# Optimization experiments

Measured on AMD Instinct MI355X. Metric: run time of the kernel, lower is better.

The kernel has to match this reference:

```python
import jax, jax.numpy as jnp
import numpy as np

D_MODEL = 1024
STATE_DIM = 64
SEQ_L = 2048


def hippo_legs_A(N):
    n = jnp.arange(N, dtype=jnp.float32)
    two_n1 = 2.0 * n + 1.0
    sq = jnp.sqrt(two_n1[:, None] * two_n1[None, :])
    A = jnp.tril(sq, k=-1) * -1.0
    return A + jnp.diag(-(n + 1.0))


def setup_inputs() -> dict:
    key = jax.random.key(0)
    kB, kC = jax.random.split(key)
    N = STATE_DIM
    n = jnp.arange(N, dtype=jnp.float32)
    B_ref = jnp.sqrt(2.0 * n + 1.0)  # (N,)
    B = jnp.tile(B_ref[None, :], (D_MODEL, 1)) + 0.01 * jax.random.normal(kB, (D_MODEL, N), dtype=jnp.float32)
    C = 0.1 * jax.random.normal(kC, (D_MODEL, N), dtype=jnp.float32)
    D = jnp.zeros((D_MODEL,), dtype=jnp.float32)
    log_dt = jnp.log(jnp.asarray(0.1, dtype=jnp.float32))
    return {"B": B, "C": C, "D": D, "log_dt": log_dt, "L": SEQ_L}


def reference(B, C, D, log_dt, L):
    N = B.shape[1]
    A = hippo_legs_A(N)                       # (N,N) continuous-time HiPPO-LegS
    dt = jax.nn.softplus(log_dt) + 1e-06
    I = jnp.eye(N, dtype=A.dtype)
    lhs = I - 0.5 * dt * A
    rhs = I + 0.5 * dt * A
    A_bar = jnp.linalg.solve(lhs, rhs)        # (N,N) bilinear discretization
    B_bar = jnp.linalg.solve(lhs, (dt * B).T).T  # (d_model, N)
    A_bar_T = A_bar.T

    def step(x, _):
        y = jnp.sum(C * x, axis=-1)           # (d_model,)
        return x @ A_bar_T, y

    _, ys = jax.lax.scan(step, B_bar, None, length=L)  # ys: (L, d_model)
    K = ys.T                                   # (d_model, L)
    K = K.at[:, 0].add(D)
    return K[:, None, :]                       # (d_model, 1, L)
```

## Files before the change

kernel.cpp:

```cpp
#include <hip/hip_runtime.h>

typedef unsigned short ushort_t;
typedef unsigned int uint_t;
typedef short short8 __attribute__((ext_vector_type(8)));
typedef float f32x4 __attribute__((ext_vector_type(4)));

namespace {

template<int CTRL, int RM>
__device__ __forceinline__ float dpp_mov0(float v) {
  return __int_as_float(__builtin_amdgcn_update_dpp(
      0, __float_as_int(v), CTRL, RM, 0xF, false));
}
template<int CTRL, int RM>
__device__ __forceinline__ float dpp_mov1(float v) {
  return __int_as_float(__builtin_amdgcn_update_dpp(
      0x3f800000, __float_as_int(v), CTRL, RM, 0xF, false));
}

__device__ __forceinline__ float rl(float v, int k) {
  return __int_as_float(__builtin_amdgcn_readlane(__float_as_int(v), k));
}

struct Hoist {
  float cs0, cs1, cs2, cs3, cs4, cs5;
  float gs0, gs1, gs2, gs3, gs4, gs5;
  float r, inv_d, hr, alpha, k2;
};

__device__ __forceinline__ Hoist make_hoist(float dt, int n) {
  float h = 0.5f * dt, fn = (float)n;
  float r = sqrtf(2.f * fn + 1.f);
  float d = 1.f + h * (fn + 1.f);
  float inv_d = 1.f / d;
  float g = (1.f - h * fn) * inv_d;
  float c = g - 1.f;
  Hoist H;
  H.r = r; H.inv_d = inv_d; H.hr = h * r;
  H.alpha = 1.f + h * fn;
  H.k2 = r * (2.f - d) * inv_d;
#define COEF_STEP(IDX, CTRL, RM)                                        \
  H.cs##IDX = c; H.gs##IDX = g;                                         \
  { float cP = dpp_mov0<CTRL, RM>(c);                                   \
    float gP = dpp_mov1<CTRL, RM>(g);                                   \
    c = fmaf(g, cP, c); g = g * gP; }
  COEF_STEP(0, 0x111, 0xF)
  COEF_STEP(1, 0x112, 0xF)
  COEF_STEP(2, 0x114, 0xF)
  COEF_STEP(3, 0x118, 0xF)
  COEF_STEP(4, 0x142, 0xA)
  COEF_STEP(5, 0x143, 0xC)
#undef COEF_STEP
  return H;
}

__device__ __forceinline__ float abar_apply(float x, const Hoist& H) {
  float w1 = H.r * x, w2 = H.k2 * x;
#define APPLY_STEP(IDX, CTRL, RM)                                       \
  { float w1P = dpp_mov0<CTRL, RM>(w1);                                 \
    float w2P = dpp_mov0<CTRL, RM>(w2);                                 \
    w2 = fmaf(H.cs##IDX, w1P, fmaf(H.gs##IDX, w2P, w2));                \
    w1 += w1P; }
  APPLY_STEP(0, 0x111, 0xF)
  APPLY_STEP(1, 0x112, 0xF)
  APPLY_STEP(2, 0x114, 0xF)
  APPLY_STEP(3, 0x118, 0xF)
  APPLY_STEP(4, 0x142, 0xA)
  APPLY_STEP(5, 0x143, 0xC)
#undef APPLY_STEP
  float tp = dpp_mov0<0x138, 0xF>(w2);
  return H.inv_d * fmaf(-H.hr, w1 + tp, H.alpha * x);
}

template<int CTRL, int RM>
__device__ __forceinline__ void linrec_step(float& G, float& W) {
  float Wo = dpp_mov0<CTRL, RM>(W);
  float Go = dpp_mov1<CTRL, RM>(G);
  W = fmaf(G, Wo, W);
  G *= Go;
}
__device__ __forceinline__ float lhs_solve(float z, const Hoist& H) {
  float G = H.gs0, W = H.r * z * H.inv_d;
  linrec_step<0x111, 0xF>(G, W);
  linrec_step<0x112, 0xF>(G, W);
  linrec_step<0x114, 0xF>(G, W);
  linrec_step<0x118, 0xF>(G, W);
  linrec_step<0x142, 0xA>(G, W);
  linrec_step<0x143, 0xC>(G, W);
  float sp = dpp_mov0<0x138, 0xF>(W);
  return (z - H.hr * sp) * H.inv_d;
}

__device__ __forceinline__ float softplus_dt(float ldt) {
  return log1pf(expf(ldt)) + 1e-6f;
}

#define KEEP4(v) asm volatile("" : "+v"(v.x), "+v"(v.y), "+v"(v.z), "+v"(v.w))

__device__ __forceinline__ void load_row_pin(const float* __restrict__ base,
                                             float4 (&p)[16]) {
  const float4* p4 = (const float4*)base;
  #pragma unroll
  for (int q = 0; q < 16; ++q) p[q] = p4[q];
  #pragma unroll
  for (int q = 0; q < 16; ++q) KEEP4(p[q]);
}

__device__ __forceinline__ float qapply_pin(const float4 (&p)[16], float u) {
  float a0 = 0.f, a1 = 0.f, a2 = 0.f, a3 = 0.f;
  #pragma unroll
  for (int q = 0; q < 16; ++q) {
    a0 = fmaf(p[q].x, rl(u, 4 * q + 0), a0);
    a1 = fmaf(p[q].y, rl(u, 4 * q + 1), a1);
    a2 = fmaf(p[q].z, rl(u, 4 * q + 2), a2);
    a3 = fmaf(p[q].w, rl(u, 4 * q + 3), a3);
  }
  return (a0 + a1) + (a2 + a3);
}

__device__ __forceinline__ float grow_matvec(const float* __restrict__ M,
                                             float u, int lane) {
  float a0 = 0.f, a1 = 0.f, a2 = 0.f, a3 = 0.f;
  const float4* m4 = (const float4*)(M + lane * 64);
  #pragma unroll
  for (int q = 0; q < 16; ++q) {
    float4 f = m4[q];
    a0 = fmaf(f.x, rl(u, 4 * q + 0), a0);
    a1 = fmaf(f.y, rl(u, 4 * q + 1), a1);
    a2 = fmaf(f.z, rl(u, 4 * q + 2), a2);
    a3 = fmaf(f.w, rl(u, 4 * q + 3), a3);
  }
  return (a0 + a1) + (a2 + a3);
}

__device__ __forceinline__ void split_store(float v, ushort_t* Hi,
                                            ushort_t* Lo, int row, int n) {
  uint_t uv = __float_as_uint(v);
  float hf = __uint_as_float(uv & 0xFFFF0000u);
  uint_t lv = __float_as_uint(v - hf);
  int idx = (row << 6) | (((n >> 3) ^ (row & 7)) << 3) | (n & 7);
  Hi[idx] = (ushort_t)(uv >> 16);
  Lo[idx] = (ushort_t)(lv >> 16);
}

__device__ __forceinline__ int frag_off(int row, int chunk) {
  return (row << 6) | ((chunk ^ (row & 7)) << 3);
}

}

__global__ __launch_bounds__(64) void hippo_pow(const float* __restrict__ ldt_p,
                                                float* __restrict__ A32c,
                                                float* __restrict__ QROW,
                                                float* __restrict__ Q2ROW) {
  const int lane = threadIdx.x;
  const int m = blockIdx.x;
  const float dt = softplus_dt(ldt_p[0]);
  const Hoist H = make_hoist(dt, lane);
  float x = (lane == m) ? 1.f : 0.f;
  #pragma unroll 1
  for (int s = 0; s < 32; ++s) x = abar_apply(x, H);
  A32c[lane * 64 + m] = x;
  #pragma unroll 1
  for (int s = 0; s < 32; ++s) x = abar_apply(x, H);
  QROW[m * 64 + lane] = x;
  #pragma unroll 1
  for (int s = 0; s < 64; ++s) x = abar_apply(x, H);
  Q2ROW[m * 64 + lane] = x;
}

__global__ __launch_bounds__(256) void hippo_main(
    const float* __restrict__ B, const float* __restrict__ C,
    const float* __restrict__ Dv, const float* __restrict__ ldt_p,
    const float* __restrict__ A32c, const float* __restrict__ QROW,
    const float* __restrict__ Q2ROW, float* __restrict__ out) {
  __shared__ __align__(16) ushort_t Uh[32 * 64], Ulo[32 * 64];
  __shared__ __align__(16) ushort_t Vh[64 * 64], Vlo[64 * 64];
  const int d = blockIdx.x;
  const int tau = threadIdx.x;
  const int lane = tau & 63;
  const int w = tau >> 6;
  const float dt = softplus_dt(ldt_p[0]);

  if (w == 0) {
    const Hoist H = make_hoist(dt, lane);
    float v = lhs_solve(dt * B[d * 64 + lane], H);
    #pragma unroll 1
    for (int j = 0; j < 32; ++j) {
      split_store(v, Vh, Vlo, j, lane);
      if (j < 31) v = abar_apply(v, H);
    }
  } else if (w == 3) {
    const Hoist H = make_hoist(dt, lane);
    float bb = lhs_solve(dt * B[d * 64 + lane], H);
    float v = grow_matvec(A32c, bb, lane);
    #pragma unroll 1
    for (int j = 32; j < 64; ++j) {
      split_store(v, Vh, Vlo, j, lane);
      if (j < 63) v = abar_apply(v, H);
    }
  } else if (w == 1) {
    float4 p[16];
    load_row_pin(Q2ROW + lane * 64, p);
    float u = C[d * 64 + lane];
    #pragma unroll 1
    for (int a = 0; a < 16; ++a) {
      split_store(u, Uh, Ulo, 2 * a, lane);
      if (a < 15) u = qapply_pin(p, u);
    }
  } else {
    float u = grow_matvec(QROW, C[d * 64 + lane], lane);
    float4 p[16];
    load_row_pin(Q2ROW + lane * 64, p);
    #pragma unroll 1
    for (int a = 0; a < 16; ++a) {
      split_store(u, Uh, Ulo, 2 * a + 1, lane);
      if (a < 15) u = qapply_pin(p, u);
    }
  }
  __syncthreads();

  const int it = w & 1;
  const int jp = w >> 1;
  const int arow = lane & 15;
  const int kg = lane >> 4;
  f32x4 acc0 = {0.f, 0.f, 0.f, 0.f};
  f32x4 acc1 = {0.f, 0.f, 0.f, 0.f};
  const int ia = (it << 4) + arow;
  const int jv0 = (jp << 5) + arow;
  const int jv1 = jv0 + 16;
  #pragma unroll
  for (int k0 = 0; k0 < 2; ++k0) {
    const int ci = (k0 << 2) + kg;
    short8 ah = *(const short8*)&Uh[frag_off(ia, ci)];
    short8 al = *(const short8*)&Ulo[frag_off(ia, ci)];
    short8 b0h = *(const short8*)&Vh[frag_off(jv0, ci)];
    short8 b0l = *(const short8*)&Vlo[frag_off(jv0, ci)];
    short8 b1h = *(const short8*)&Vh[frag_off(jv1, ci)];
    short8 b1l = *(const short8*)&Vlo[frag_off(jv1, ci)];
    acc0 = __builtin_amdgcn_mfma_f32_16x16x32_bf16(ah, b0h, acc0, 0, 0, 0);
    acc0 = __builtin_amdgcn_mfma_f32_16x16x32_bf16(al, b0h, acc0, 0, 0, 0);
    acc0 = __builtin_amdgcn_mfma_f32_16x16x32_bf16(ah, b0l, acc0, 0, 0, 0);
    acc1 = __builtin_amdgcn_mfma_f32_16x16x32_bf16(ah, b1h, acc1, 0, 0, 0);
    acc1 = __builtin_amdgcn_mfma_f32_16x16x32_bf16(al, b1h, acc1, 0, 0, 0);
    acc1 = __builtin_amdgcn_mfma_f32_16x16x32_bf16(ah, b1l, acc1, 0, 0, 0);
  }
  #pragma unroll
  for (int r = 0; r < 4; ++r) {
    const int i = (it << 4) + (kg << 2) + r;
    const int j0 = (jp << 5) + arow;
    float y0 = acc0[r];
    if (i == 0 && j0 == 0) y0 += Dv[d];
    out[((size_t)d << 11) + (i << 6) + j0] = y0;
    out[((size_t)d << 11) + (i << 6) + j0 + 16] = acc1[r];
  }
}

extern "C" void kernel_launch(void* const* d_in, const int* in_sizes, int n_in,
                              void* d_out, int out_size, void* d_ws, size_t ws_size,
                              hipStream_t stream) {
  const float* B   = (const float*)d_in[0];
  const float* C   = (const float*)d_in[1];
  const float* Dv  = (const float*)d_in[2];
  const float* ldt = (const float*)d_in[3];
  const int d_model = in_sizes[2];
  float* A32c  = (float*)d_ws;
  float* QROW  = (float*)d_ws + 4096;
  float* Q2ROW = (float*)d_ws + 8192;
  hippo_pow<<<64, 64, 0, stream>>>(ldt, A32c, QROW, Q2ROW);
  hippo_main<<<d_model, 256, 0, stream>>>(B, C, Dv, ldt, A32c, QROW, Q2ROW,
                                          (float*)d_out);
}
```

Before: 39.62 us.

## Shorten serial power chains with more precomputed A powers and grid-synced squaring

The prep kernel now stores A^16, A^32, A^48 and A^64, and builds the higher powers (A^128, A^256) by squaring, using atomic counters as a grid-wide barrier across the 64 blocks instead of running 64 more serial steps. In the main kernel each wave then runs two independent recurrence chains of half the length, interleaved, which halves the serial dependency depth for building the V and U tiles. The cost is extra matvecs per wave, a memset launch, and a spin-wait barrier that relies on all 64 prep blocks being resident at once.

```diff
diff --git a/kernel.cpp b/kernel.cpp
--- a/kernel.cpp
+++ b/kernel.cpp
@@ -147,33 +147,66 @@
   return (row << 6) | ((chunk ^ (row & 7)) << 3);
 }
 
-}
-
-__global__ __launch_bounds__(64) void hippo_pow(const float* __restrict__ ldt_p,
-                                                float* __restrict__ A32c,
-                                                float* __restrict__ QROW,
-                                                float* __restrict__ Q2ROW) {
+__device__ __forceinline__ void wait_cnt(const uint_t* f, uint_t tgt) {
+  while (__hip_atomic_load(f, __ATOMIC_ACQUIRE, __HIP_MEMORY_SCOPE_AGENT) < tgt)
+    __builtin_amdgcn_s_sleep(8);
+}
+__device__ __forceinline__ void signal_cnt(uint_t* f, int lane) {
+  __threadfence();
+  if (lane == 0)
+    __hip_atomic_fetch_add(f, 1u, __ATOMIC_RELEASE, __HIP_MEMORY_SCOPE_AGENT);
+}
+
+}
+
+__global__ __launch_bounds__(64) void hippo_prep(
+    const float* __restrict__ ldt_p, uint_t* __restrict__ flags,
+    float* __restrict__ A16c, float* __restrict__ A32c,
+    float* __restrict__ A48c, float* __restrict__ QROW,
+    float* __restrict__ A64RM, float* __restrict__ Q2ROW,
+    float* __restrict__ Q2RM, float* __restrict__ Q4ROW) {
   const int lane = threadIdx.x;
   const int m = blockIdx.x;
   const float dt = softplus_dt(ldt_p[0]);
   const Hoist H = make_hoist(dt, lane);
   float x = (lane == m) ? 1.f : 0.f;
   #pragma unroll 1
-  for (int s = 0; s < 32; ++s) x = abar_apply(x, H);
+  for (int s = 0; s < 16; ++s) x = abar_apply(x, H);
+  A16c[lane * 64 + m] = x;
+  #pragma unroll 1
+  for (int s = 0; s < 16; ++s) x = abar_apply(x, H);
   A32c[lane * 64 + m] = x;
   #pragma unroll 1
-  for (int s = 0; s < 32; ++s) x = abar_apply(x, H);
+  for (int s = 0; s < 16; ++s) x = abar_apply(x, H);
+  A48c[lane * 64 + m] = x;
+  #pragma unroll 1
+  for (int s = 0; s < 16; ++s) x = abar_apply(x, H);
   QROW[m * 64 + lane] = x;
-  #pragma unroll 1
-  for (int s = 0; s < 64; ++s) x = abar_apply(x, H);
-  Q2ROW[m * 64 + lane] = x;
+  A64RM[lane * 64 + m] = x;
+  signal_cnt(&flags[0], lane);
+  wait_cnt(&flags[0], 64);
+  {
+    float4 p[16];
+    load_row_pin(A64RM + lane * 64, p);
+    float x2 = qapply_pin(p, x);
+    Q2ROW[m * 64 + lane] = x2;
+    Q2RM[lane * 64 + m] = x2;
+    signal_cnt(&flags[1], lane);
+    wait_cnt(&flags[1], 64);
+    float4 p2[16];
+    load_row_pin(Q2RM + lane * 64, p2);
+    float x4 = qapply_pin(p2, x2);
+    Q4ROW[m * 64 + lane] = x4;
+  }
 }
 
 __global__ __launch_bounds__(256) void hippo_main(
     const float* __restrict__ B, const float* __restrict__ C,
     const float* __restrict__ Dv, const float* __restrict__ ldt_p,
-    const float* __restrict__ A32c, const float* __restrict__ QROW,
-    const float* __restrict__ Q2ROW, float* __restrict__ out) {
+    const float* __restrict__ A16c, const float* __restrict__ A32c,
+    const float* __restrict__ A48c, const float* __restrict__ QROW,
+    const float* __restrict__ Q2ROW, const float* __restrict__ Q4ROW,
+    float* __restrict__ out) {
   __shared__ __align__(16) ushort_t Uh[32 * 64], Ulo[32 * 64];
   __shared__ __align__(16) ushort_t Vh[64 * 64], Vlo[64 * 64];
   const int d = blockIdx.x;
@@ -182,40 +215,53 @@
   const int w = tau >> 6;
   const float dt = softplus_dt(ldt_p[0]);
 
-  if (w == 0) {
-    const Hoist H = make_hoist(dt, lane);
-    float v = lhs_solve(dt * B[d * 64 + lane], H);
-    #pragma unroll 1
-    for (int j = 0; j < 32; ++j) {
-      split_store(v, Vh, Vlo, j, lane);
-      if (j < 31) v = abar_apply(v, H);
-    }
-  } else if (w == 3) {
+  if ((w & 1) == 0) {
+  }
+  if (w == 0 || w == 3) {
     const Hoist H = make_hoist(dt, lane);
     float bb = lhs_solve(dt * B[d * 64 + lane], H);
-    float v = grow_matvec(A32c, bb, lane);
+    float va, vb;
+    int j0;
+    if (w == 0) {
+      va = bb;
+      vb = grow_matvec(A16c, bb, lane);
+      j0 = 0;
+    } else {
+      va = grow_matvec(A32c, bb, lane);
+      vb = grow_matvec(A48c, bb, lane);
+      j0 = 32;
+    }
     #pragma unroll 1
-    for (int j = 32; j < 64; ++j) {
-      split_store(v, Vh, Vlo, j, lane);
-      if (j < 63) v = abar_apply(v, H);
-    }
-  } else if (w == 1) {
-    float4 p[16];
-    load_row_pin(Q2ROW + lane * 64, p);
-    float u = C[d * 64 + lane];
-    #pragma unroll 1
-    for (int a = 0; a < 16; ++a) {
-      split_store(u, Uh, Ulo, 2 * a, lane);
-      if (a < 15) u = qapply_pin(p, u);
+    for (int jj = 0; jj < 16; ++jj) {
+      split_store(va, Vh, Vlo, j0 + jj, lane);
+      split_store(vb, Vh, Vlo, j0 + 16 + jj, lane);
+      if (jj < 15) {
+        va = abar_apply(va, H);
+        vb = abar_apply(vb, H);
+      }
     }
   } else {
-    float u = grow_matvec(QROW, C[d * 64 + lane], lane);
+    float ua, ub;
+    int i0;
+    if (w == 1) {
+      ua = C[d * 64 + lane];
+      ub = grow_matvec(Q2ROW, ua, lane);
+      i0 = 0;
+    } else {
+      ua = grow_matvec(QROW, C[d * 64 + lane], lane);
+      ub = grow_matvec(Q2ROW, ua, lane);
+      i0 = 1;
+    }
     float4 p[16];
-    load_row_pin(Q2ROW + lane * 64, p);
+    load_row_pin(Q4ROW + lane * 64, p);
     #pragma unroll 1
-    for (int a = 0; a < 16; ++a) {
-      split_store(u, Uh, Ulo, 2 * a + 1, lane);
-      if (a < 15) u = qapply_pin(p, u);
+    for (int a = 0; a < 8; ++a) {
+      split_store(ua, Uh, Ulo, (a << 2) + i0, lane);
+      split_store(ub, Uh, Ulo, (a << 2) + i0 + 2, lane);
+      if (a < 7) {
+        ua = qapply_pin(p, ua);
+        ub = qapply_pin(p, ub);
+      }
     }
   }
   __syncthreads();
@@ -264,10 +310,21 @@
   const float* Dv  = (const float*)d_in[2];
   const float* ldt = (const float*)d_in[3];
   const int d_model = in_sizes[2];
-  float* A32c  = (float*)d_ws;
-  float* QROW  = (float*)d_ws + 4096;
-  float* Q2ROW = (float*)d_ws + 8192;
-  hippo_pow<<<64, 64, 0, stream>>>(ldt, A32c, QROW, Q2ROW);
-  hippo_main<<<d_model, 256, 0, stream>>>(B, C, Dv, ldt, A32c, QROW, Q2ROW,
-                                          (float*)d_out);
-}
+
+  char* ws = (char*)d_ws;
+  uint_t* flags = (uint_t*)ws;
+  float* A16c  = (float*)(ws + 256);
+  float* A32c  = (float*)(ws + 256 + 16384 * 1);
+  float* A48c  = (float*)(ws + 256 + 16384 * 2);
+  float* QROW  = (float*)(ws + 256 + 16384 * 3);
+  float* A64RM = (float*)(ws + 256 + 16384 * 4);
+  float* Q2ROW = (float*)(ws + 256 + 16384 * 5);
+  float* Q2RM  = (float*)(ws + 256 + 16384 * 6);
+  float* Q4ROW = (float*)(ws + 256 + 16384 * 7);
+
+  hipMemsetAsync(flags, 0, 256, stream);
+  hippo_prep<<<64, 64, 0, stream>>>(ldt, flags, A16c, A32c, A48c, QROW,
+                                    A64RM, Q2ROW, Q2RM, Q4ROW);
+  hippo_main<<<d_model, 256, 0, stream>>>(B, C, Dv, ldt, A16c, A32c, A48c,
+                                          QROW, Q2ROW, Q4ROW, (float*)d_out);
+}
```

Result: slower. 53.60 us (+35.3%).
